# Optimization experiments

Measured on AMD Instinct MI355X. Metric: run time of the kernel, lower is better.

The kernel has to match this reference:

```python
import jax, jax.numpy as jnp
import numpy as np

B, S, D = 256, 64, 512
H, DK, DV = 8, 64, 64
DFF = 2048
IN_SIZE = S * D  # 32768
OUT = 50
EPS = 1e-5


def _layernorm(x, gamma, beta):
    mu = jnp.mean(x, axis=-1, keepdims=True)
    var = jnp.mean((x - mu) ** 2, axis=-1, keepdims=True)
    return (x - mu) * jax.lax.rsqrt(var + EPS) * gamma + beta


def setup_inputs() -> dict:
    key = jax.random.key(0)
    ks = jax.random.split(key, 16)
    s = lambda fan_in: 1.0 / np.sqrt(fan_in)
    inp = {
        "inputs": jax.random.normal(ks[0], (B, S, D), dtype=jnp.float32),
        # per-head projections stacked over heads (concat order preserved)
        "Wq": jax.random.normal(ks[1], (H, D, DK), dtype=jnp.float32) * s(D),
        "bq": jnp.zeros((H, DK), dtype=jnp.float32),
        "Wk": jax.random.normal(ks[2], (H, D, DK), dtype=jnp.float32) * s(D),
        "bk": jnp.zeros((H, DK), dtype=jnp.float32),
        "Wv": jax.random.normal(ks[3], (H, D, DV), dtype=jnp.float32) * s(D),
        "bv": jnp.zeros((H, DV), dtype=jnp.float32),
        "Wo": jax.random.normal(ks[4], (H * DV, D), dtype=jnp.float32) * s(H * DV),
        "bo": jnp.zeros((D,), dtype=jnp.float32),
        "ln1_g": jnp.ones((D,), dtype=jnp.float32),
        "ln1_b": jnp.zeros((D,), dtype=jnp.float32),
        "W1": jax.random.normal(ks[5], (IN_SIZE, DFF), dtype=jnp.float32) * s(IN_SIZE),
        "b1": jnp.zeros((DFF,), dtype=jnp.float32),
        "W2": jax.random.normal(ks[6], (DFF, IN_SIZE), dtype=jnp.float32) * s(DFF),
        "b2": jnp.zeros((IN_SIZE,), dtype=jnp.float32),
        "ln2_g": jnp.ones((IN_SIZE,), dtype=jnp.float32),
        "ln2_b": jnp.zeros((IN_SIZE,), dtype=jnp.float32),
        "Wf": jax.random.normal(ks[7], (IN_SIZE, OUT), dtype=jnp.float32) * s(IN_SIZE),
        "bf": jnp.zeros((OUT,), dtype=jnp.float32),
    }
    return inp


def reference(inputs, Wq, bq, Wk, bk, Wv, bv, Wo, bo, ln1_g, ln1_b,
              W1, b1, W2, b2, ln2_g, ln2_b, Wf, bf):
    # --- multi-head attention (all heads batched via einsum) ---
    q = jnp.einsum('bsd,hdk->bhsk', inputs, Wq) + bq[:, None, :]
    k = jnp.einsum('bsd,hdk->bhsk', inputs, Wk) + bk[:, None, :]
    v = jnp.einsum('bsd,hdv->bhsv', inputs, Wv) + bv[:, None, :]
    scores = jnp.einsum('bhsk,bhtk->bhst', q, k) / jnp.sqrt(jnp.float32(DK))
    attn = jax.nn.softmax(scores, axis=-1)
    ctx = jnp.einsum('bhst,bhtv->bhsv', attn, v)          # [B,H,S,DV]
    ctx = ctx.transpose(0, 2, 1, 3).reshape(B, S, H * DV)  # concat heads
    proj = ctx @ Wo + bo
    hs = _layernorm(inputs + proj, ln1_g, ln1_b)           # [B,S,D]
    # --- flatten + FFN with residual + LN ---
    x = hs.reshape(B, IN_SIZE)
    h = jax.nn.relu(x @ W1 + b1)
    y = _layernorm(h @ W2 + b2 + x, ln2_g, ln2_b)
    # --- final classifier ---
    return y @ Wf + bf
```

## Files before the change

kernel.cpp:

```cpp
#include <hip/hip_runtime.h>

#define BB   256
#define SS   64
#define DD   512
#define HH   8
#define DKK  64
#define BSZ  16384
#define INSZ 32768
#define DFF  2048
#define NOUT 50
#define KSF  128
#define KCF  256

typedef float f32x4 __attribute__((ext_vector_type(4)));
typedef __bf16 bf16x8 __attribute__((ext_vector_type(8)));
typedef unsigned short u16x8 __attribute__((ext_vector_type(8)));

__device__ inline unsigned short f2bf(float f) {
    unsigned u = __builtin_bit_cast(unsigned, f);
    u += 0x7FFFu + ((u >> 16) & 1u);
    return (unsigned short)(u >> 16);
}
__device__ inline bf16x8 ld_frag(const unsigned short* p) {
    return __builtin_bit_cast(bf16x8, *(const u16x8*)p);
}
#define MFMA(a,b,c) __builtin_amdgcn_mfma_f32_16x16x32_bf16(a,b,c,0,0,0)

__global__ __launch_bounds__(256) void k_qkv(
    const float* __restrict__ X,  const float* __restrict__ Wq,
    const float* __restrict__ bq, const float* __restrict__ Wk,
    const float* __restrict__ bk, const float* __restrict__ Wv,
    const float* __restrict__ bv, unsigned short* __restrict__ qkv)
{
    const int mt = blockIdx.x, h = blockIdx.y;
    const int tid = threadIdx.x, wave = tid >> 6, lane = tid & 63;
    const int m0 = mt * 64;
    __shared__ unsigned short Xs[64][72];
    __shared__ unsigned short Ws[192][72];

    const float* Wb0 = Wq + (size_t)h * DD * DKK;
    const float* Wb1 = Wk + (size_t)h * DD * DKK;
    const float* Wb2 = Wv + (size_t)h * DD * DKK;

    f32x4 acc[12] = {};
    for (int k0 = 0; k0 < DD; k0 += 64) {
        for (int p = 0; p < 4; ++p) {
            int e = tid + p * 256;
            int r = e >> 4, c4 = e & 15;
            float4 v = *(const float4*)(X + (size_t)(m0 + r) * DD + k0 + c4 * 4);
            int c = c4 * 4;
            Xs[r][c] = f2bf(v.x); Xs[r][c+1] = f2bf(v.y);
            Xs[r][c+2] = f2bf(v.z); Xs[r][c+3] = f2bf(v.w);
        }
        for (int w3 = 0; w3 < 3; ++w3) {
            const float* W = (w3 == 0) ? Wb0 : (w3 == 1) ? Wb1 : Wb2;
            for (int p = 0; p < 4; ++p) {
                int e = tid + p * 256;
                int kr = e >> 4, c4 = e & 15;
                float4 v = *(const float4*)(W + (size_t)(k0 + kr) * DKK + c4 * 4);
                int nb = w3 * 64 + c4 * 4;
                Ws[nb][kr] = f2bf(v.x); Ws[nb+1][kr] = f2bf(v.y);
                Ws[nb+2][kr] = f2bf(v.z); Ws[nb+3][kr] = f2bf(v.w);
            }
        }
        __syncthreads();
        for (int ks = 0; ks < 64; ks += 32) {
            bf16x8 a = ld_frag(&Xs[wave*16 + (lane & 15)][ks + (lane >> 4) * 8]);
            for (int nt = 0; nt < 12; ++nt) {
                bf16x8 b = ld_frag(&Ws[nt*16 + (lane & 15)][ks + (lane >> 4) * 8]);
                acc[nt] = MFMA(a, b, acc[nt]);
            }
        }
        __syncthreads();
    }
    for (int nt = 0; nt < 12; ++nt) {
        int w3 = nt >> 2;
        const float* bias = ((w3 == 0) ? bq : (w3 == 1) ? bk : bv) + h * DKK;
        float scale = (w3 == 0) ? 0.125f : 1.0f;
        unsigned short* out = qkv + ((size_t)(w3 * BB + mt) * HH + h) * (SS * DKK);
        for (int r = 0; r < 4; ++r) {
            int s = wave * 16 + (lane >> 4) * 4 + r;
            int c = (nt & 3) * 16 + (lane & 15);
            out[s * DKK + c] = f2bf((acc[nt][r] + bias[c]) * scale);
        }
    }
}

__global__ __launch_bounds__(256) void k_attn(
    const unsigned short* __restrict__ qkv, unsigned short* __restrict__ ctx)
{
    const int b = blockIdx.x >> 3, h = blockIdx.x & 7;
    const int tid = threadIdx.x, wave = tid >> 6, lane = tid & 63;
    __shared__ unsigned short Qs[64][72], Ks[64][72], Vt[64][72], Ps[64][72];

    const unsigned short* qp = qkv + ((size_t)(0 * BB + b) * HH + h) * 4096;
    const unsigned short* kp = qkv + ((size_t)(1 * BB + b) * HH + h) * 4096;
    const unsigned short* vp = qkv + ((size_t)(2 * BB + b) * HH + h) * 4096;

    for (int p = 0; p < 4; ++p) {
        int e = tid + p * 256;
        int r = e >> 4, c4 = (e & 15) * 4;
        *(ushort4*)&Qs[r][c4] = *(const ushort4*)(qp + r * 64 + c4);
        *(ushort4*)&Ks[r][c4] = *(const ushort4*)(kp + r * 64 + c4);
    }
    for (int p = 0; p < 16; ++p) {
        int e = tid + p * 256;
        int t = e >> 6, dv = e & 63;
        Vt[dv][t] = vp[t * 64 + dv];
    }
    __syncthreads();

    f32x4 sa[4] = {};
    for (int ks = 0; ks < 64; ks += 32) {
        bf16x8 a = ld_frag(&Qs[wave*16 + (lane & 15)][ks + (lane >> 4) * 8]);
        for (int nt = 0; nt < 4; ++nt) {
            bf16x8 bb = ld_frag(&Ks[nt*16 + (lane & 15)][ks + (lane >> 4) * 8]);
            sa[nt] = MFMA(a, bb, sa[nt]);
        }
    }
    for (int r = 0; r < 4; ++r) {
        float mx = fmaxf(fmaxf(sa[0][r], sa[1][r]), fmaxf(sa[2][r], sa[3][r]));
        for (int off = 1; off < 16; off <<= 1) mx = fmaxf(mx, __shfl_xor(mx, off, 64));
        float e0 = __expf(sa[0][r] - mx), e1 = __expf(sa[1][r] - mx);
        float e2 = __expf(sa[2][r] - mx), e3 = __expf(sa[3][r] - mx);
        float sm = e0 + e1 + e2 + e3;
        for (int off = 1; off < 16; off <<= 1) sm += __shfl_xor(sm, off, 64);
        float inv = 1.f / sm;
        sa[0][r] = e0 * inv; sa[1][r] = e1 * inv; sa[2][r] = e2 * inv; sa[3][r] = e3 * inv;
    }
    for (int nt = 0; nt < 4; ++nt)
        for (int r = 0; r < 4; ++r)
            Ps[wave*16 + (lane >> 4) * 4 + r][nt*16 + (lane & 15)] = f2bf(sa[nt][r]);
    __syncthreads();

    f32x4 oa[4] = {};
    for (int ks = 0; ks < 64; ks += 32) {
        bf16x8 a = ld_frag(&Ps[wave*16 + (lane & 15)][ks + (lane >> 4) * 8]);
        for (int nt = 0; nt < 4; ++nt) {
            bf16x8 bb = ld_frag(&Vt[nt*16 + (lane & 15)][ks + (lane >> 4) * 8]);
            oa[nt] = MFMA(a, bb, oa[nt]);
        }
    }
    unsigned short* cp = ctx + (size_t)b * SS * DD + h * DKK;
    for (int nt = 0; nt < 4; ++nt)
        for (int r = 0; r < 4; ++r) {
            int s = wave * 16 + (lane >> 4) * 4 + r;
            int dv = nt * 16 + (lane & 15);
            cp[(size_t)s * DD + dv] = f2bf(oa[nt][r]);
        }
}

__global__ __launch_bounds__(256) void k_oproj(
    const unsigned short* __restrict__ ctx, const float* __restrict__ Wo,
    const float* __restrict__ bo, const float* __restrict__ X,
    float* __restrict__ t1)
{
    const int mt = blockIdx.x, n0 = blockIdx.y * 128;
    const int tid = threadIdx.x, wave = tid >> 6, lane = tid & 63;
    const int m0 = mt * 64;
    __shared__ unsigned short As[64][72], Bs[128][72];
    f32x4 acc[8] = {};
    for (int k0 = 0; k0 < DD; k0 += 64) {
        for (int p = 0; p < 4; ++p) {
            int e = tid + p * 256; int r = e >> 4, c4 = (e & 15) * 4;
            *(ushort4*)&As[r][c4] = *(const ushort4*)(ctx + (size_t)(m0 + r) * DD + k0 + c4);
        }
        for (int p = 0; p < 8; ++p) {
            int e = tid + p * 256; int kr = e >> 5, c4 = e & 31;
            float4 v = *(const float4*)(Wo + (size_t)(k0 + kr) * DD + n0 + c4 * 4);
            int nb = c4 * 4;
            Bs[nb][kr] = f2bf(v.x); Bs[nb+1][kr] = f2bf(v.y);
            Bs[nb+2][kr] = f2bf(v.z); Bs[nb+3][kr] = f2bf(v.w);
        }
        __syncthreads();
        for (int ks = 0; ks < 64; ks += 32) {
            bf16x8 a = ld_frag(&As[wave*16 + (lane & 15)][ks + (lane >> 4) * 8]);
            for (int nt = 0; nt < 8; ++nt) {
                bf16x8 bb = ld_frag(&Bs[nt*16 + (lane & 15)][ks + (lane >> 4) * 8]);
                acc[nt] = MFMA(a, bb, acc[nt]);
            }
        }
        __syncthreads();
    }
    for (int nt = 0; nt < 8; ++nt)
        for (int r = 0; r < 4; ++r) {
            int m = m0 + wave * 16 + (lane >> 4) * 4 + r;
            int n = n0 + nt * 16 + (lane & 15);
            t1[(size_t)m * DD + n] = acc[nt][r] + bo[n] + X[(size_t)m * DD + n];
        }
}

__global__ __launch_bounds__(256) void k_ln1(
    float* __restrict__ t1, const float* __restrict__ g,
    const float* __restrict__ bv, unsigned short* __restrict__ hs16)
{
    const int tid = threadIdx.x, wave = tid >> 6, lane = tid & 63;
    const int row = blockIdx.x * 4 + wave;
    float* p = t1 + (size_t)row * DD;
    float4 v0 = *(const float4*)(p + lane * 4);
    float4 v1 = *(const float4*)(p + 256 + lane * 4);
    float s = v0.x + v0.y + v0.z + v0.w + v1.x + v1.y + v1.z + v1.w;
    float q = v0.x*v0.x + v0.y*v0.y + v0.z*v0.z + v0.w*v0.w
            + v1.x*v1.x + v1.y*v1.y + v1.z*v1.z + v1.w*v1.w;
    for (int off = 1; off < 64; off <<= 1) { s += __shfl_xor(s, off, 64); q += __shfl_xor(q, off, 64); }
    float mu = s / DD;
    float rs = rsqrtf(q / DD - mu * mu + 1e-5f);
    float4 g0 = *(const float4*)(g + lane * 4), g1 = *(const float4*)(g + 256 + lane * 4);
    float4 b0 = *(const float4*)(bv + lane * 4), b1 = *(const float4*)(bv + 256 + lane * 4);
    float4 o0, o1;
    o0.x = (v0.x - mu) * rs * g0.x + b0.x; o0.y = (v0.y - mu) * rs * g0.y + b0.y;
    o0.z = (v0.z - mu) * rs * g0.z + b0.z; o0.w = (v0.w - mu) * rs * g0.w + b0.w;
    o1.x = (v1.x - mu) * rs * g1.x + b1.x; o1.y = (v1.y - mu) * rs * g1.y + b1.y;
    o1.z = (v1.z - mu) * rs * g1.z + b1.z; o1.w = (v1.w - mu) * rs * g1.w + b1.w;
    *(float4*)(p + lane * 4) = o0;
    *(float4*)(p + 256 + lane * 4) = o1;
    unsigned short* hp = hs16 + (size_t)row * DD;
    ushort4 u;
    u.x = f2bf(o0.x); u.y = f2bf(o0.y); u.z = f2bf(o0.z); u.w = f2bf(o0.w);
    *(ushort4*)(hp + lane * 4) = u;
    u.x = f2bf(o1.x); u.y = f2bf(o1.y); u.z = f2bf(o1.z); u.w = f2bf(o1.w);
    *(ushort4*)(hp + 256 + lane * 4) = u;
}

__global__ __launch_bounds__(256) void k_ffn1(
    const unsigned short* __restrict__ hs16, const float* __restrict__ W1,
    float* __restrict__ part)
{
    const int n0 = blockIdx.x * 64, kbase = blockIdx.y * 2048;
    const int tid = threadIdx.x, wave = tid >> 6, lane = tid & 63;
    __shared__ unsigned short As[256][72], Bs[64][72];
    f32x4 acc[4][4] = {};
    for (int kc = 0; kc < 2048; kc += 64) {
        int k0 = kbase + kc;
        for (int p = 0; p < 16; ++p) {
            int e = tid + p * 256; int r = e >> 4, c4 = (e & 15) * 4;
            *(ushort4*)&As[r][c4] = *(const ushort4*)(hs16 + (size_t)r * INSZ + k0 + c4);
        }
        for (int p = 0; p < 4; ++p) {
            int e = tid + p * 256; int kr = e >> 4, c4 = e & 15;
            float4 v = *(const float4*)(W1 + (size_t)(k0 + kr) * DFF + n0 + c4 * 4);
            int nb = c4 * 4;
            Bs[nb][kr] = f2bf(v.x); Bs[nb+1][kr] = f2bf(v.y);
            Bs[nb+2][kr] = f2bf(v.z); Bs[nb+3][kr] = f2bf(v.w);
        }
        __syncthreads();
        for (int ks = 0; ks < 64; ks += 32) {
            bf16x8 bfr[4];
            for (int nt = 0; nt < 4; ++nt)
                bfr[nt] = ld_frag(&Bs[nt*16 + (lane & 15)][ks + (lane >> 4) * 8]);
            for (int mt2 = 0; mt2 < 4; ++mt2) {
                bf16x8 a = ld_frag(&As[wave*64 + mt2*16 + (lane & 15)][ks + (lane >> 4) * 8]);
                for (int nt = 0; nt < 4; ++nt) acc[mt2][nt] = MFMA(a, bfr[nt], acc[mt2][nt]);
            }
        }
        __syncthreads();
    }
    float* pp = part + (size_t)blockIdx.y * 256 * DFF;
    for (int mt2 = 0; mt2 < 4; ++mt2)
        for (int nt = 0; nt < 4; ++nt)
            for (int r = 0; r < 4; ++r) {
                int m = wave * 64 + mt2 * 16 + (lane >> 4) * 4 + r;
                int n = n0 + nt * 16 + (lane & 15);
                pp[(size_t)m * DFF + n] = acc[mt2][nt][r];
            }
}

__global__ __launch_bounds__(256) void k_ffn1red(
    const float* __restrict__ part, const float* __restrict__ b1,
    unsigned short* __restrict__ h16)
{
    int e = blockIdx.x * 256 + threadIdx.x;
    int m = e >> 9;
    int c = (e & 511) * 4;
    float4 s = {0.f, 0.f, 0.f, 0.f};
    for (int p = 0; p < 16; ++p) {
        float4 v = *(const float4*)(part + ((size_t)p * 256 + m) * DFF + c);
        s.x += v.x; s.y += v.y; s.z += v.z; s.w += v.w;
    }
    float4 bb = *(const float4*)(b1 + c);
    s.x = fmaxf(s.x + bb.x, 0.f); s.y = fmaxf(s.y + bb.y, 0.f);
    s.z = fmaxf(s.z + bb.z, 0.f); s.w = fmaxf(s.w + bb.w, 0.f);
    ushort4 u; u.x = f2bf(s.x); u.y = f2bf(s.y); u.z = f2bf(s.z); u.w = f2bf(s.w);
    *(ushort4*)(h16 + (size_t)m * DFF + c) = u;
}

__global__ __launch_bounds__(256) void k_ffn2(
    const unsigned short* __restrict__ h16, const float* __restrict__ W2,
    const float* __restrict__ b2, const float* __restrict__ hs32,
    float* __restrict__ t2)
{
    const int n0 = blockIdx.x * 64;
    const int tid = threadIdx.x, wave = tid >> 6, lane = tid & 63;
    __shared__ unsigned short As[256][72], Bs[64][72];
    f32x4 acc[4][4] = {};
    for (int k0 = 0; k0 < DFF; k0 += 64) {
        for (int p = 0; p < 16; ++p) {
            int e = tid + p * 256; int r = e >> 4, c4 = (e & 15) * 4;
            *(ushort4*)&As[r][c4] = *(const ushort4*)(h16 + (size_t)r * DFF + k0 + c4);
        }
        for (int p = 0; p < 4; ++p) {
            int e = tid + p * 256; int kr = e >> 4, c4 = e & 15;
            float4 v = *(const float4*)(W2 + (size_t)(k0 + kr) * INSZ + n0 + c4 * 4);
            int nb = c4 * 4;
            Bs[nb][kr] = f2bf(v.x); Bs[nb+1][kr] = f2bf(v.y);
            Bs[nb+2][kr] = f2bf(v.z); Bs[nb+3][kr] = f2bf(v.w);
        }
        __syncthreads();
        for (int ks = 0; ks < 64; ks += 32) {
            bf16x8 bfr[4];
            for (int nt = 0; nt < 4; ++nt)
                bfr[nt] = ld_frag(&Bs[nt*16 + (lane & 15)][ks + (lane >> 4) * 8]);
            for (int mt2 = 0; mt2 < 4; ++mt2) {
                bf16x8 a = ld_frag(&As[wave*64 + mt2*16 + (lane & 15)][ks + (lane >> 4) * 8]);
                for (int nt = 0; nt < 4; ++nt) acc[mt2][nt] = MFMA(a, bfr[nt], acc[mt2][nt]);
            }
        }
        __syncthreads();
    }
    for (int mt2 = 0; mt2 < 4; ++mt2)
        for (int nt = 0; nt < 4; ++nt)
            for (int r = 0; r < 4; ++r) {
                int m = wave * 64 + mt2 * 16 + (lane >> 4) * 4 + r;
                int n = n0 + nt * 16 + (lane & 15);
                size_t idx = (size_t)m * INSZ + n;
                t2[idx] = acc[mt2][nt][r] + b2[n] + hs32[idx];
            }
}

__global__ __launch_bounds__(256) void k_ln2stats(
    const float* __restrict__ t2, float* __restrict__ stats)
{
    const int m = blockIdx.x, tid = threadIdx.x;
    const float* p = t2 + (size_t)m * INSZ;
    float s = 0.f, q = 0.f;
    for (int i = tid; i < INSZ / 4; i += 256) {
        float4 v = *(const float4*)(p + i * 4);
        s += v.x + v.y + v.z + v.w;
        q += v.x*v.x + v.y*v.y + v.z*v.z + v.w*v.w;
    }
    for (int off = 1; off < 64; off <<= 1) { s += __shfl_xor(s, off, 64); q += __shfl_xor(q, off, 64); }
    __shared__ float ss[4], qq[4];
    if ((tid & 63) == 0) { ss[tid >> 6] = s; qq[tid >> 6] = q; }
    __syncthreads();
    if (tid == 0) {
        s = ss[0] + ss[1] + ss[2] + ss[3];
        q = qq[0] + qq[1] + qq[2] + qq[3];
        float mu = s / INSZ;
        stats[m * 2] = mu;
        stats[m * 2 + 1] = rsqrtf(q / INSZ - mu * mu + 1e-5f);
    }
}

__global__ __launch_bounds__(256) void k_fgemm(
    const float* __restrict__ t2, const float* __restrict__ g,
    const float* __restrict__ bv, const float* __restrict__ Wf,
    float* __restrict__ fpart)
{
    const int sp = blockIdx.x, kbase = sp * KCF;
    const int tid = threadIdx.x, wave = tid >> 6, lane = tid & 63;
    __shared__ unsigned short As[272][72], Bs[64][72];
    f32x4 acc[5][4] = {};
    for (int kc = 0; kc < KCF; kc += 64) {
        int k0 = kbase + kc;
        for (int p = 0; p < 68; ++p) {
            int e = tid + p * 256;
            int r = e >> 6, c = e & 63;
            int k = k0 + c;
            float val;
            if (r < 256)      val = t2[(size_t)r * INSZ + k] * g[k];
            else if (r == 256) val = g[k];
            else if (r == 257) val = bv[k];
            else               val = 0.f;
            As[r][c] = f2bf(val);
        }
        for (int p = 0; p < 16; ++p) {
            int e = tid + p * 256;
            int kr = e >> 6, n = e & 63;
            Bs[n][kr] = (n < NOUT) ? f2bf(Wf[(size_t)(k0 + kr) * NOUT + n]) : (unsigned short)0;
        }
        __syncthreads();
        for (int ks = 0; ks < 64; ks += 32) {
            bf16x8 bfr[4];
            for (int nt = 0; nt < 4; ++nt)
                bfr[nt] = ld_frag(&Bs[nt*16 + (lane & 15)][ks + (lane >> 4) * 8]);
            int i = 0;
            for (int mt = wave; mt < 17; mt += 4, ++i) {
                bf16x8 a = ld_frag(&As[mt*16 + (lane & 15)][ks + (lane >> 4) * 8]);
                for (int nt = 0; nt < 4; ++nt) acc[i][nt] = MFMA(a, bfr[nt], acc[i][nt]);
            }
        }
        __syncthreads();
    }
    float* pp = fpart + (size_t)sp * 272 * 64;
    int i = 0;
    for (int mt = wave; mt < 17; mt += 4, ++i)
        for (int nt = 0; nt < 4; ++nt)
            for (int r = 0; r < 4; ++r) {
                int m = mt * 16 + (lane >> 4) * 4 + r;
                int n = nt * 16 + (lane & 15);
                pp[m * 64 + n] = acc[i][nt][r];
            }
}

__global__ __launch_bounds__(64) void k_fout(
    const float* __restrict__ fpart, const float* __restrict__ stats,
    const float* __restrict__ bf_, float* __restrict__ out)
{
    const int m = blockIdx.x, n = threadIdx.x;
    float s = 0.f, sg = 0.f, sb = 0.f;
    for (int sp = 0; sp < KSF; ++sp) {
        const float* pp = fpart + (size_t)sp * 272 * 64;
        s  += pp[m * 64 + n];
        sg += pp[256 * 64 + n];
        sb += pp[257 * 64 + n];
    }
    if (n < NOUT) {
        float mu = stats[m * 2], rs = stats[m * 2 + 1];
        out[m * NOUT + n] = rs * (s - mu * sg) + sb + bf_[n];
    }
}

extern "C" void kernel_launch(void* const* d_in, const int* in_sizes, int n_in,
                              void* d_out, int out_size, void* d_ws, size_t ws_size,
                              hipStream_t stream) {
    const float* X   = (const float*)d_in[0];
    const float* Wq  = (const float*)d_in[1];
    const float* bq  = (const float*)d_in[2];
    const float* Wk  = (const float*)d_in[3];
    const float* bk  = (const float*)d_in[4];
    const float* Wv  = (const float*)d_in[5];
    const float* bv  = (const float*)d_in[6];
    const float* Wo  = (const float*)d_in[7];
    const float* bo  = (const float*)d_in[8];
    const float* g1  = (const float*)d_in[9];
    const float* b1v = (const float*)d_in[10];
    const float* W1  = (const float*)d_in[11];
    const float* b1  = (const float*)d_in[12];
    const float* W2  = (const float*)d_in[13];
    const float* b2  = (const float*)d_in[14];
    const float* g2  = (const float*)d_in[15];
    const float* b2v = (const float*)d_in[16];
    const float* Wf  = (const float*)d_in[17];
    const float* bfv = (const float*)d_in[18];
    float* out = (float*)d_out;
    char* ws = (char*)d_ws;

    unsigned short* qkv  = (unsigned short*)(ws + 0);
    float* part1         = (float*)(ws + 0);
    float* fpart         = (float*)(ws + 0);
    unsigned short* hs16 = (unsigned short*)(ws + 33554432);
    unsigned short* ctx  = (unsigned short*)(ws + 50331648);
    float* t2            = (float*)(ws + 50331648);
    float* t1            = (float*)(ws + 83886080);
    unsigned short* h16  = (unsigned short*)(ws + 117440512);
    float* stats         = (float*)(ws + 118489088);

    k_qkv<<<dim3(256, 8), 256, 0, stream>>>(X, Wq, bq, Wk, bk, Wv, bv, qkv);
    k_attn<<<2048, 256, 0, stream>>>(qkv, ctx);
    k_oproj<<<dim3(256, 4), 256, 0, stream>>>(ctx, Wo, bo, X, t1);
    k_ln1<<<4096, 256, 0, stream>>>(t1, g1, b1v, hs16);
    k_ffn1<<<dim3(32, 16), 256, 0, stream>>>(hs16, W1, part1);
    k_ffn1red<<<512, 256, 0, stream>>>(part1, b1, h16);
    k_ffn2<<<512, 256, 0, stream>>>(h16, W2, b2, t1, t2);
    k_ln2stats<<<256, 256, 0, stream>>>(t2, stats);
    k_fgemm<<<KSF, 256, 0, stream>>>(t2, g2, b2v, Wf, fpart);
    k_fout<<<256, 64, 0, stream>>>(fpart, stats, bfv, out);
}
```

Baseline: 1.029 ms.

## Swizzle LDS tiles, retile QKV/oproj GEMMs, pre-convert X, rework final split-K

```diff
diff --git a/kernel.cpp b/kernel.cpp
--- a/kernel.cpp
+++ b/kernel.cpp
@@ -9,8 +9,8 @@
 #define INSZ 32768
 #define DFF  2048
 #define NOUT 50
-#define KSF  128
-#define KCF  256
+#define KSF  256
+#define KCF  128
 
 typedef float f32x4 __attribute__((ext_vector_type(4)));
 typedef __bf16 bf16x8 __attribute__((ext_vector_type(8)));
@@ -26,64 +26,93 @@
 }
 #define MFMA(a,b,c) __builtin_amdgcn_mfma_f32_16x16x32_bf16(a,b,c,0,0,0)
 
+__device__ inline int sw(int row, int col) {
+    return row * 64 + ((((col >> 3) ^ (row & 7)) << 3) | (col & 7));
+}
+
+__device__ inline void stage_w64(const float* __restrict__ W, int ldn,
+                                 unsigned short* Bs, int tid) {
+    const int n = tid & 63, wq = tid >> 6;
+    #pragma unroll
+    for (int p = 0; p < 2; ++p) {
+        const int k0 = wq * 8 + p * 32;
+        const float* src = W + (size_t)k0 * ldn + n;
+        unsigned short tmp[8];
+        #pragma unroll
+        for (int j = 0; j < 8; ++j) tmp[j] = f2bf(src[(size_t)j * ldn]);
+        *(u16x8*)&Bs[sw(n, k0)] = *(const u16x8*)tmp;
+    }
+}
+
+__device__ inline void stage_a256(const unsigned short* __restrict__ src, int lds_,
+                                  unsigned short* As, int tid) {
+    #pragma unroll
+    for (int p = 0; p < 8; ++p) {
+        int e = tid + p * 256;
+        int r = e >> 3, c8 = (e & 7) * 8;
+        u16x8 v = *(const u16x8*)(src + (size_t)r * lds_ + c8);
+        *(u16x8*)&As[sw(r, c8)] = v;
+    }
+}
+
+__global__ __launch_bounds__(256) void k_x16(
+    const float* __restrict__ X, unsigned short* __restrict__ x16)
+{
+    int e = blockIdx.x * 256 + threadIdx.x;
+    float4 v = ((const float4*)X)[e];
+    ushort4 u;
+    u.x = f2bf(v.x); u.y = f2bf(v.y); u.z = f2bf(v.z); u.w = f2bf(v.w);
+    ((ushort4*)x16)[e] = u;
+}
+
 __global__ __launch_bounds__(256) void k_qkv(
-    const float* __restrict__ X,  const float* __restrict__ Wq,
-    const float* __restrict__ bq, const float* __restrict__ Wk,
-    const float* __restrict__ bk, const float* __restrict__ Wv,
-    const float* __restrict__ bv, unsigned short* __restrict__ qkv)
-{
-    const int mt = blockIdx.x, h = blockIdx.y;
-    const int tid = threadIdx.x, wave = tid >> 6, lane = tid & 63;
-    const int m0 = mt * 64;
-    __shared__ unsigned short Xs[64][72];
-    __shared__ unsigned short Ws[192][72];
-
-    const float* Wb0 = Wq + (size_t)h * DD * DKK;
-    const float* Wb1 = Wk + (size_t)h * DD * DKK;
-    const float* Wb2 = Wv + (size_t)h * DD * DKK;
-
-    f32x4 acc[12] = {};
+    const unsigned short* __restrict__ x16,
+    const float* __restrict__ Wq, const float* __restrict__ bq,
+    const float* __restrict__ Wk, const float* __restrict__ bk,
+    const float* __restrict__ Wv, const float* __restrict__ bv,
+    unsigned short* __restrict__ qkv)
+{
+    const int m0 = blockIdx.x * 256;
+    const int nt = blockIdx.y, w3 = nt >> 3, h = nt & 7;
+    const int tid = threadIdx.x, wave = tid >> 6, lane = tid & 63;
+    const float* Wbase = ((w3 == 0) ? Wq : (w3 == 1) ? Wk : Wv) + (size_t)h * DD * DKK;
+    __shared__ __align__(16) unsigned short As[256 * 64];
+    __shared__ __align__(16) unsigned short Bs[64 * 64];
+
+    f32x4 acc[4][4] = {};
     for (int k0 = 0; k0 < DD; k0 += 64) {
-        for (int p = 0; p < 4; ++p) {
-            int e = tid + p * 256;
-            int r = e >> 4, c4 = e & 15;
-            float4 v = *(const float4*)(X + (size_t)(m0 + r) * DD + k0 + c4 * 4);
-            int c = c4 * 4;
-            Xs[r][c] = f2bf(v.x); Xs[r][c+1] = f2bf(v.y);
-            Xs[r][c+2] = f2bf(v.z); Xs[r][c+3] = f2bf(v.w);
-        }
-        for (int w3 = 0; w3 < 3; ++w3) {
-            const float* W = (w3 == 0) ? Wb0 : (w3 == 1) ? Wb1 : Wb2;
-            for (int p = 0; p < 4; ++p) {
-                int e = tid + p * 256;
-                int kr = e >> 4, c4 = e & 15;
-                float4 v = *(const float4*)(W + (size_t)(k0 + kr) * DKK + c4 * 4);
-                int nb = w3 * 64 + c4 * 4;
-                Ws[nb][kr] = f2bf(v.x); Ws[nb+1][kr] = f2bf(v.y);
-                Ws[nb+2][kr] = f2bf(v.z); Ws[nb+3][kr] = f2bf(v.w);
-            }
-        }
-        __syncthreads();
+        stage_a256(x16 + (size_t)m0 * DD + k0, DD, As, tid);
+        stage_w64(Wbase + (size_t)k0 * DKK, DKK, Bs, tid);
+        __syncthreads();
+        #pragma unroll
         for (int ks = 0; ks < 64; ks += 32) {
-            bf16x8 a = ld_frag(&Xs[wave*16 + (lane & 15)][ks + (lane >> 4) * 8]);
-            for (int nt = 0; nt < 12; ++nt) {
-                bf16x8 b = ld_frag(&Ws[nt*16 + (lane & 15)][ks + (lane >> 4) * 8]);
-                acc[nt] = MFMA(a, b, acc[nt]);
-            }
-        }
-        __syncthreads();
-    }
-    for (int nt = 0; nt < 12; ++nt) {
-        int w3 = nt >> 2;
-        const float* bias = ((w3 == 0) ? bq : (w3 == 1) ? bk : bv) + h * DKK;
-        float scale = (w3 == 0) ? 0.125f : 1.0f;
-        unsigned short* out = qkv + ((size_t)(w3 * BB + mt) * HH + h) * (SS * DKK);
-        for (int r = 0; r < 4; ++r) {
-            int s = wave * 16 + (lane >> 4) * 4 + r;
-            int c = (nt & 3) * 16 + (lane & 15);
-            out[s * DKK + c] = f2bf((acc[nt][r] + bias[c]) * scale);
-        }
-    }
+            bf16x8 bfr[4];
+            #pragma unroll
+            for (int n2 = 0; n2 < 4; ++n2)
+                bfr[n2] = ld_frag(&Bs[sw(n2*16 + (lane & 15), ks + (lane >> 4) * 8)]);
+            #pragma unroll
+            for (int m2 = 0; m2 < 4; ++m2) {
+                bf16x8 a = ld_frag(&As[sw(wave*64 + m2*16 + (lane & 15), ks + (lane >> 4) * 8)]);
+                #pragma unroll
+                for (int n2 = 0; n2 < 4; ++n2) acc[m2][n2] = MFMA(a, bfr[n2], acc[m2][n2]);
+            }
+        }
+        __syncthreads();
+    }
+    const float* bias = ((w3 == 0) ? bq : (w3 == 1) ? bk : bv) + h * DKK;
+    const float scale = (w3 == 0) ? 0.125f : 1.0f;
+    #pragma unroll
+    for (int m2 = 0; m2 < 4; ++m2)
+        #pragma unroll
+        for (int n2 = 0; n2 < 4; ++n2)
+            #pragma unroll
+            for (int r = 0; r < 4; ++r) {
+                int m = m0 + wave*64 + m2*16 + (lane >> 4) * 4 + r;
+                int b = m >> 6, s = m & 63;
+                int dk = n2*16 + (lane & 15);
+                qkv[((size_t)(w3 * BB + b) * HH + h) * 4096 + s * 64 + dk]
+                    = f2bf((acc[m2][n2][r] + bias[dk]) * scale);
+            }
 }
 
 __global__ __launch_bounds__(256) void k_attn(
@@ -91,33 +120,40 @@
 {
     const int b = blockIdx.x >> 3, h = blockIdx.x & 7;
     const int tid = threadIdx.x, wave = tid >> 6, lane = tid & 63;
-    __shared__ unsigned short Qs[64][72], Ks[64][72], Vt[64][72], Ps[64][72];
+    __shared__ __align__(16) unsigned short Qs[64*64], Ks[64*64], Vt[64*64], Ps[64*64];
 
     const unsigned short* qp = qkv + ((size_t)(0 * BB + b) * HH + h) * 4096;
     const unsigned short* kp = qkv + ((size_t)(1 * BB + b) * HH + h) * 4096;
     const unsigned short* vp = qkv + ((size_t)(2 * BB + b) * HH + h) * 4096;
 
-    for (int p = 0; p < 4; ++p) {
+    #pragma unroll
+    for (int p = 0; p < 2; ++p) {
         int e = tid + p * 256;
-        int r = e >> 4, c4 = (e & 15) * 4;
-        *(ushort4*)&Qs[r][c4] = *(const ushort4*)(qp + r * 64 + c4);
-        *(ushort4*)&Ks[r][c4] = *(const ushort4*)(kp + r * 64 + c4);
-    }
-    for (int p = 0; p < 16; ++p) {
-        int e = tid + p * 256;
-        int t = e >> 6, dv = e & 63;
-        Vt[dv][t] = vp[t * 64 + dv];
+        int r = e >> 3, c8 = (e & 7) * 8;
+        *(u16x8*)&Qs[sw(r, c8)] = *(const u16x8*)(qp + r * 64 + c8);
+        *(u16x8*)&Ks[sw(r, c8)] = *(const u16x8*)(kp + r * 64 + c8);
+    }
+    {
+        int dv = tid & 63, tb = (tid >> 6) * 16;
+        unsigned short tmp[16];
+        #pragma unroll
+        for (int i = 0; i < 16; ++i) tmp[i] = vp[(tb + i) * 64 + dv];
+        *(u16x8*)&Vt[sw(dv, tb)]     = *(const u16x8*)&tmp[0];
+        *(u16x8*)&Vt[sw(dv, tb + 8)] = *(const u16x8*)&tmp[8];
     }
     __syncthreads();
 
     f32x4 sa[4] = {};
+    #pragma unroll
     for (int ks = 0; ks < 64; ks += 32) {
-        bf16x8 a = ld_frag(&Qs[wave*16 + (lane & 15)][ks + (lane >> 4) * 8]);
-        for (int nt = 0; nt < 4; ++nt) {
-            bf16x8 bb = ld_frag(&Ks[nt*16 + (lane & 15)][ks + (lane >> 4) * 8]);
-            sa[nt] = MFMA(a, bb, sa[nt]);
-        }
-    }
+        bf16x8 a = ld_frag(&Qs[sw(wave*16 + (lane & 15), ks + (lane >> 4) * 8)]);
+        #pragma unroll
+        for (int n2 = 0; n2 < 4; ++n2) {
+            bf16x8 bb = ld_frag(&Ks[sw(n2*16 + (lane & 15), ks + (lane >> 4) * 8)]);
+            sa[n2] = MFMA(a, bb, sa[n2]);
+        }
+    }
+    #pragma unroll
     for (int r = 0; r < 4; ++r) {
         float mx = fmaxf(fmaxf(sa[0][r], sa[1][r]), fmaxf(sa[2][r], sa[3][r]));
         for (int off = 1; off < 16; off <<= 1) mx = fmaxf(mx, __shfl_xor(mx, off, 64));
@@ -128,25 +164,30 @@
         float inv = 1.f / sm;
         sa[0][r] = e0 * inv; sa[1][r] = e1 * inv; sa[2][r] = e2 * inv; sa[3][r] = e3 * inv;
     }
-    for (int nt = 0; nt < 4; ++nt)
+    #pragma unroll
+    for (int n2 = 0; n2 < 4; ++n2)
+        #pragma unroll
         for (int r = 0; r < 4; ++r)
-            Ps[wave*16 + (lane >> 4) * 4 + r][nt*16 + (lane & 15)] = f2bf(sa[nt][r]);
+            Ps[sw(wave*16 + (lane >> 4)*4 + r, n2*16 + (lane & 15))] = f2bf(sa[n2][r]);
     __syncthreads();
 
     f32x4 oa[4] = {};
+    #pragma unroll
     for (int ks = 0; ks < 64; ks += 32) {
-        bf16x8 a = ld_frag(&Ps[wave*16 + (lane & 15)][ks + (lane >> 4) * 8]);
-        for (int nt = 0; nt < 4; ++nt) {
-            bf16x8 bb = ld_frag(&Vt[nt*16 + (lane & 15)][ks + (lane >> 4) * 8]);
-            oa[nt] = MFMA(a, bb, oa[nt]);
+        bf16x8 a = ld_frag(&Ps[sw(wave*16 + (lane & 15), ks + (lane >> 4) * 8)]);
+        #pragma unroll
+        for (int n2 = 0; n2 < 4; ++n2) {
+            bf16x8 bb = ld_frag(&Vt[sw(n2*16 + (lane & 15), ks + (lane >> 4) * 8)]);
+            oa[n2] = MFMA(a, bb, oa[n2]);
         }
     }
     unsigned short* cp = ctx + (size_t)b * SS * DD + h * DKK;
-    for (int nt = 0; nt < 4; ++nt)
+    #pragma unroll
+    for (int n2 = 0; n2 < 4; ++n2)
+        #pragma unroll
         for (int r = 0; r < 4; ++r) {
-            int s = wave * 16 + (lane >> 4) * 4 + r;
-            int dv = nt * 16 + (lane & 15);
-            cp[(size_t)s * DD + dv] = f2bf(oa[nt][r]);
+            int s = wave*16 + (lane >> 4)*4 + r;
+            cp[(size_t)s * DD + n2*16 + (lane & 15)] = f2bf(oa[n2][r]);
         }
 }
 
@@ -155,39 +196,40 @@
     const float* __restrict__ bo, const float* __restrict__ X,
     float* __restrict__ t1)
 {
-    const int mt = blockIdx.x, n0 = blockIdx.y * 128;
-    const int tid = threadIdx.x, wave = tid >> 6, lane = tid & 63;
-    const int m0 = mt * 64;
-    __shared__ unsigned short As[64][72], Bs[128][72];
-    f32x4 acc[8] = {};
+    const int m0 = blockIdx.x * 256, n0 = blockIdx.y * 64;
+    const int tid = threadIdx.x, wave = tid >> 6, lane = tid & 63;
+    __shared__ __align__(16) unsigned short As[256 * 64];
+    __shared__ __align__(16) unsigned short Bs[64 * 64];
+    f32x4 acc[4][4] = {};
     for (int k0 = 0; k0 < DD; k0 += 64) {
-        for (int p = 0; p < 4; ++p) {
-            int e = tid + p * 256; int r = e >> 4, c4 = (e & 15) * 4;
-            *(ushort4*)&As[r][c4] = *(const ushort4*)(ctx + (size_t)(m0 + r) * DD + k0 + c4);
-        }
-        for (int p = 0; p < 8; ++p) {
-            int e = tid + p * 256; int kr = e >> 5, c4 = e & 31;
-            float4 v = *(const float4*)(Wo + (size_t)(k0 + kr) * DD + n0 + c4 * 4);
-            int nb = c4 * 4;
-            Bs[nb][kr] = f2bf(v.x); Bs[nb+1][kr] = f2bf(v.y);
-            Bs[nb+2][kr] = f2bf(v.z); Bs[nb+3][kr] = f2bf(v.w);
-        }
-        __syncthreads();
+        stage_a256(ctx + (size_t)m0 * DD + k0, DD, As, tid);
+        stage_w64(Wo + (size_t)k0 * DD + n0, DD, Bs, tid);
+        __syncthreads();
+        #pragma unroll
         for (int ks = 0; ks < 64; ks += 32) {
-            bf16x8 a = ld_frag(&As[wave*16 + (lane & 15)][ks + (lane >> 4) * 8]);
-            for (int nt = 0; nt < 8; ++nt) {
-                bf16x8 bb = ld_frag(&Bs[nt*16 + (lane & 15)][ks + (lane >> 4) * 8]);
-                acc[nt] = MFMA(a, bb, acc[nt]);
-            }
-        }
-        __syncthreads();
-    }
-    for (int nt = 0; nt < 8; ++nt)
-        for (int r = 0; r < 4; ++r) {
-            int m = m0 + wave * 16 + (lane >> 4) * 4 + r;
-            int n = n0 + nt * 16 + (lane & 15);
-            t1[(size_t)m * DD + n] = acc[nt][r] + bo[n] + X[(size_t)m * DD + n];
-        }
+            bf16x8 bfr[4];
+            #pragma unroll
+            for (int n2 = 0; n2 < 4; ++n2)
+                bfr[n2] = ld_frag(&Bs[sw(n2*16 + (lane & 15), ks + (lane >> 4) * 8)]);
+            #pragma unroll
+            for (int m2 = 0; m2 < 4; ++m2) {
+                bf16x8 a = ld_frag(&As[sw(wave*64 + m2*16 + (lane & 15), ks + (lane >> 4) * 8)]);
+                #pragma unroll
+                for (int n2 = 0; n2 < 4; ++n2) acc[m2][n2] = MFMA(a, bfr[n2], acc[m2][n2]);
+            }
+        }
+        __syncthreads();
+    }
+    #pragma unroll
+    for (int m2 = 0; m2 < 4; ++m2)
+        #pragma unroll
+        for (int n2 = 0; n2 < 4; ++n2)
+            #pragma unroll
+            for (int r = 0; r < 4; ++r) {
+                int m = m0 + wave*64 + m2*16 + (lane >> 4)*4 + r;
+                int n = n0 + n2*16 + (lane & 15);
+                t1[(size_t)m * DD + n] = acc[m2][n2][r] + bo[n] + X[(size_t)m * DD + n];
+            }
 }
 
 __global__ __launch_bounds__(256) void k_ln1(
@@ -228,40 +270,39 @@
 {
     const int n0 = blockIdx.x * 64, kbase = blockIdx.y * 2048;
     const int tid = threadIdx.x, wave = tid >> 6, lane = tid & 63;
-    __shared__ unsigned short As[256][72], Bs[64][72];
+    __shared__ __align__(16) unsigned short As[256 * 64];
+    __shared__ __align__(16) unsigned short Bs[64 * 64];
     f32x4 acc[4][4] = {};
     for (int kc = 0; kc < 2048; kc += 64) {
         int k0 = kbase + kc;
-        for (int p = 0; p < 16; ++p) {
-            int e = tid + p * 256; int r = e >> 4, c4 = (e & 15) * 4;
-            *(ushort4*)&As[r][c4] = *(const ushort4*)(hs16 + (size_t)r * INSZ + k0 + c4);
-        }
-        for (int p = 0; p < 4; ++p) {
-            int e = tid + p * 256; int kr = e >> 4, c4 = e & 15;
-            float4 v = *(const float4*)(W1 + (size_t)(k0 + kr) * DFF + n0 + c4 * 4);
-            int nb = c4 * 4;
-            Bs[nb][kr] = f2bf(v.x); Bs[nb+1][kr] = f2bf(v.y);
-            Bs[nb+2][kr] = f2bf(v.z); Bs[nb+3][kr] = f2bf(v.w);
-        }
-        __syncthreads();
+        stage_a256(hs16 + k0, INSZ, As, tid);
+        stage_w64(W1 + (size_t)k0 * DFF + n0, DFF, Bs, tid);
+        __syncthreads();
+        #pragma unroll
         for (int ks = 0; ks < 64; ks += 32) {
             bf16x8 bfr[4];
-            for (int nt = 0; nt < 4; ++nt)
-                bfr[nt] = ld_frag(&Bs[nt*16 + (lane & 15)][ks + (lane >> 4) * 8]);
-            for (int mt2 = 0; mt2 < 4; ++mt2) {
-                bf16x8 a = ld_frag(&As[wave*64 + mt2*16 + (lane & 15)][ks + (lane >> 4) * 8]);
-                for (int nt = 0; nt < 4; ++nt) acc[mt2][nt] = MFMA(a, bfr[nt], acc[mt2][nt]);
+            #pragma unroll
+            for (int n2 = 0; n2 < 4; ++n2)
+                bfr[n2] = ld_frag(&Bs[sw(n2*16 + (lane & 15), ks + (lane >> 4) * 8)]);
+            #pragma unroll
+            for (int m2 = 0; m2 < 4; ++m2) {
+                bf16x8 a = ld_frag(&As[sw(wave*64 + m2*16 + (lane & 15), ks + (lane >> 4) * 8)]);
+                #pragma unroll
+                for (int n2 = 0; n2 < 4; ++n2) acc[m2][n2] = MFMA(a, bfr[n2], acc[m2][n2]);
             }
         }
         __syncthreads();
     }
     float* pp = part + (size_t)blockIdx.y * 256 * DFF;
-    for (int mt2 = 0; mt2 < 4; ++mt2)
-        for (int nt = 0; nt < 4; ++nt)
+    #pragma unroll
+    for (int m2 = 0; m2 < 4; ++m2)
+        #pragma unroll
+        for (int n2 = 0; n2 < 4; ++n2)
+            #pragma unroll
             for (int r = 0; r < 4; ++r) {
-                int m = wave * 64 + mt2 * 16 + (lane >> 4) * 4 + r;
-                int n = n0 + nt * 16 + (lane & 15);
-                pp[(size_t)m * DFF + n] = acc[mt2][nt][r];
+                int m = wave*64 + m2*16 + (lane >> 4)*4 + r;
+                int n = n0 + n2*16 + (lane & 15);
+                pp[(size_t)m * DFF + n] = acc[m2][n2][r];
             }
 }
 
@@ -291,39 +332,38 @@
 {
     const int n0 = blockIdx.x * 64;
     const int tid = threadIdx.x, wave = tid >> 6, lane = tid & 63;
-    __shared__ unsigned short As[256][72], Bs[64][72];
+    __shared__ __align__(16) unsigned short As[256 * 64];
+    __shared__ __align__(16) unsigned short Bs[64 * 64];
     f32x4 acc[4][4] = {};
     for (int k0 = 0; k0 < DFF; k0 += 64) {
-        for (int p = 0; p < 16; ++p) {
-            int e = tid + p * 256; int r = e >> 4, c4 = (e & 15) * 4;
-            *(ushort4*)&As[r][c4] = *(const ushort4*)(h16 + (size_t)r * DFF + k0 + c4);
-        }
-        for (int p = 0; p < 4; ++p) {
-            int e = tid + p * 256; int kr = e >> 4, c4 = e & 15;
-            float4 v = *(const float4*)(W2 + (size_t)(k0 + kr) * INSZ + n0 + c4 * 4);
-            int nb = c4 * 4;
-            Bs[nb][kr] = f2bf(v.x); Bs[nb+1][kr] = f2bf(v.y);
-            Bs[nb+2][kr] = f2bf(v.z); Bs[nb+3][kr] = f2bf(v.w);
-        }
-        __syncthreads();
+        stage_a256(h16 + k0, DFF, As, tid);
+        stage_w64(W2 + (size_t)k0 * INSZ + n0, INSZ, Bs, tid);
+        __syncthreads();
+        #pragma unroll
         for (int ks = 0; ks < 64; ks += 32) {
             bf16x8 bfr[4];
-            for (int nt = 0; nt < 4; ++nt)
-                bfr[nt] = ld_frag(&Bs[nt*16 + (lane & 15)][ks + (lane >> 4) * 8]);
-            for (int mt2 = 0; mt2 < 4; ++mt2) {
-                bf16x8 a = ld_frag(&As[wave*64 + mt2*16 + (lane & 15)][ks + (lane >> 4) * 8]);
-                for (int nt = 0; nt < 4; ++nt) acc[mt2][nt] = MFMA(a, bfr[nt], acc[mt2][nt]);
-            }
-        }
-        __syncthreads();
-    }
-    for (int mt2 = 0; mt2 < 4; ++mt2)
-        for (int nt = 0; nt < 4; ++nt)
+            #pragma unroll
+            for (int n2 = 0; n2 < 4; ++n2)
+                bfr[n2] = ld_frag(&Bs[sw(n2*16 + (lane & 15), ks + (lane >> 4) * 8)]);
+            #pragma unroll
+            for (int m2 = 0; m2 < 4; ++m2) {
+                bf16x8 a = ld_frag(&As[sw(wave*64 + m2*16 + (lane & 15), ks + (lane >> 4) * 8)]);
+                #pragma unroll
+                for (int n2 = 0; n2 < 4; ++n2) acc[m2][n2] = MFMA(a, bfr[n2], acc[m2][n2]);
+            }
+        }
+        __syncthreads();
+    }
+    #pragma unroll
+    for (int m2 = 0; m2 < 4; ++m2)
+        #pragma unroll
+        for (int n2 = 0; n2 < 4; ++n2)
+            #pragma unroll
             for (int r = 0; r < 4; ++r) {
-                int m = wave * 64 + mt2 * 16 + (lane >> 4) * 4 + r;
-                int n = n0 + nt * 16 + (lane & 15);
+                int m = wave*64 + m2*16 + (lane >> 4)*4 + r;
+                int n = n0 + n2*16 + (lane & 15);
                 size_t idx = (size_t)m * INSZ + n;
-                t2[idx] = acc[mt2][nt][r] + b2[n] + hs32[idx];
+                t2[idx] = acc[m2][n2][r] + b2[n] + hs32[idx];
             }
 }
 
@@ -358,7 +398,8 @@
 {
     const int sp = blockIdx.x, kbase = sp * KCF;
     const int tid = threadIdx.x, wave = tid >> 6, lane = tid & 63;
-    __shared__ unsigned short As[272][72], Bs[64][72];
+    __shared__ __align__(16) unsigned short As[272][72];
+    __shared__ __align__(16) unsigned short Bs[64 * 64];
     f32x4 acc[5][4] = {};
     for (int kc = 0; kc < KCF; kc += 64) {
         int k0 = kbase + kc;
@@ -367,56 +408,73 @@
             int r = e >> 6, c = e & 63;
             int k = k0 + c;
             float val;
-            if (r < 256)      val = t2[(size_t)r * INSZ + k] * g[k];
+            if (r < 256)       val = t2[(size_t)r * INSZ + k] * g[k];
             else if (r == 256) val = g[k];
             else if (r == 257) val = bv[k];
             else               val = 0.f;
             As[r][c] = f2bf(val);
         }
-        for (int p = 0; p < 16; ++p) {
-            int e = tid + p * 256;
-            int kr = e >> 6, n = e & 63;
-            Bs[n][kr] = (n < NOUT) ? f2bf(Wf[(size_t)(k0 + kr) * NOUT + n]) : (unsigned short)0;
-        }
-        __syncthreads();
+        {
+            int n = tid & 63, wq = tid >> 6;
+            #pragma unroll
+            for (int p = 0; p < 2; ++p) {
+                int kk = wq * 8 + p * 32;
+                unsigned short tmp[8];
+                #pragma unroll
+                for (int j = 0; j < 8; ++j)
+                    tmp[j] = (n < NOUT) ? f2bf(Wf[(size_t)(k0 + kk + j) * NOUT + n]) : (unsigned short)0;
+                *(u16x8*)&Bs[sw(n, kk)] = *(const u16x8*)tmp;
+            }
+        }
+        __syncthreads();
+        #pragma unroll
         for (int ks = 0; ks < 64; ks += 32) {
             bf16x8 bfr[4];
-            for (int nt = 0; nt < 4; ++nt)
-                bfr[nt] = ld_frag(&Bs[nt*16 + (lane & 15)][ks + (lane >> 4) * 8]);
+            #pragma unroll
+            for (int n2 = 0; n2 < 4; ++n2)
+                bfr[n2] = ld_frag(&Bs[sw(n2*16 + (lane & 15), ks + (lane >> 4) * 8)]);
             int i = 0;
             for (int mt = wave; mt < 17; mt += 4, ++i) {
                 bf16x8 a = ld_frag(&As[mt*16 + (lane & 15)][ks + (lane >> 4) * 8]);
-                for (int nt = 0; nt < 4; ++nt) acc[i][nt] = MFMA(a, bfr[nt], acc[i][nt]);
-            }
-        }
-        __syncthreads();
-    }
-    float* pp = fpart + (size_t)sp * 272 * 64;
+                #pragma unroll
+                for (int n2 = 0; n2 < 4; ++n2) acc[i][n2] = MFMA(a, bfr[n2], acc[i][n2]);
+            }
+        }
+        __syncthreads();
+    }
     int i = 0;
     for (int mt = wave; mt < 17; mt += 4, ++i)
-        for (int nt = 0; nt < 4; ++nt)
+        #pragma unroll
+        for (int n2 = 0; n2 < 4; ++n2)
+            #pragma unroll
             for (int r = 0; r < 4; ++r) {
-                int m = mt * 16 + (lane >> 4) * 4 + r;
-                int n = nt * 16 + (lane & 15);
-                pp[m * 64 + n] = acc[i][nt][r];
-            }
-}
-
-__global__ __launch_bounds__(64) void k_fout(
+                int m = mt*16 + (lane >> 4)*4 + r;
+                int n = n2*16 + (lane & 15);
+                fpart[((size_t)m * KSF + sp) * 64 + n] = acc[i][n2][r];
+            }
+}
+
+__global__ __launch_bounds__(256) void k_fout(
     const float* __restrict__ fpart, const float* __restrict__ stats,
     const float* __restrict__ bf_, float* __restrict__ out)
 {
-    const int m = blockIdx.x, n = threadIdx.x;
+    const int m = blockIdx.x, tid = threadIdx.x;
+    const int n = tid & 63, sq = tid >> 6;
     float s = 0.f, sg = 0.f, sb = 0.f;
-    for (int sp = 0; sp < KSF; ++sp) {
-        const float* pp = fpart + (size_t)sp * 272 * 64;
-        s  += pp[m * 64 + n];
-        sg += pp[256 * 64 + n];
-        sb += pp[257 * 64 + n];
-    }
-    if (n < NOUT) {
-        float mu = stats[m * 2], rs = stats[m * 2 + 1];
-        out[m * NOUT + n] = rs * (s - mu * sg) + sb + bf_[n];
+    for (int sp = sq * 64; sp < sq * 64 + 64; ++sp) {
+        s  += fpart[((size_t)m   * KSF + sp) * 64 + n];
+        sg += fpart[((size_t)256 * KSF + sp) * 64 + n];
+        sb += fpart[((size_t)257 * KSF + sp) * 64 + n];
+    }
+    __shared__ float red[3][4][64];
+    red[0][sq][n] = s; red[1][sq][n] = sg; red[2][sq][n] = sb;
+    __syncthreads();
+    if (tid < NOUT) {
+        float S  = red[0][0][tid] + red[0][1][tid] + red[0][2][tid] + red[0][3][tid];
+        float SG = red[1][0][tid] + red[1][1][tid] + red[1][2][tid] + red[1][3][tid];
+        float SB = red[2][0][tid] + red[2][1][tid] + red[2][2][tid] + red[2][3][tid];
+        float mu = stats[m * 2], rv = stats[m * 2 + 1];
+        out[m * NOUT + tid] = rv * (S - mu * SG) + SB + bf_[tid];
     }
 }
 
@@ -445,24 +503,26 @@
     float* out = (float*)d_out;
     char* ws = (char*)d_ws;
 
-    unsigned short* qkv  = (unsigned short*)(ws + 0);
-    float* part1         = (float*)(ws + 0);
-    float* fpart         = (float*)(ws + 0);
-    unsigned short* hs16 = (unsigned short*)(ws + 33554432);
-    unsigned short* ctx  = (unsigned short*)(ws + 50331648);
-    float* t2            = (float*)(ws + 50331648);
+    unsigned short* x16  = (unsigned short*)(ws + 0);
+    unsigned short* qkv  = (unsigned short*)(ws + 16777216);
+    unsigned short* ctx  = (unsigned short*)(ws + 67108864);
     float* t1            = (float*)(ws + 83886080);
-    unsigned short* h16  = (unsigned short*)(ws + 117440512);
-    float* stats         = (float*)(ws + 118489088);
-
-    k_qkv<<<dim3(256, 8), 256, 0, stream>>>(X, Wq, bq, Wk, bk, Wv, bv, qkv);
+    unsigned short* hs16 = (unsigned short*)(ws + 0);
+    float* part1         = (float*)(ws + 16777216);
+    unsigned short* h16  = (unsigned short*)(ws + 50331648);
+    float* t2            = (float*)(ws + 0);
+    float* fpart         = (float*)(ws + 33554432);
+    float* stats         = (float*)(ws + 51380224);
+
+    k_x16<<<8192, 256, 0, stream>>>(X, x16);
+    k_qkv<<<dim3(64, 24), 256, 0, stream>>>(x16, Wq, bq, Wk, bk, Wv, bv, qkv);
     k_attn<<<2048, 256, 0, stream>>>(qkv, ctx);
-    k_oproj<<<dim3(256, 4), 256, 0, stream>>>(ctx, Wo, bo, X, t1);
+    k_oproj<<<dim3(64, 8), 256, 0, stream>>>(ctx, Wo, bo, X, t1);
     k_ln1<<<4096, 256, 0, stream>>>(t1, g1, b1v, hs16);
     k_ffn1<<<dim3(32, 16), 256, 0, stream>>>(hs16, W1, part1);
     k_ffn1red<<<512, 256, 0, stream>>>(part1, b1, h16);
     k_ffn2<<<512, 256, 0, stream>>>(h16, W2, b2, t1, t2);
     k_ln2stats<<<256, 256, 0, stream>>>(t2, stats);
     k_fgemm<<<KSF, 256, 0, stream>>>(t2, g2, b2v, Wf, fpart);
-    k_fout<<<256, 64, 0, stream>>>(fpart, stats, bfv, out);
-}
+    k_fout<<<256, 256, 0, stream>>>(fpart, stats, bfv, out);
+}
```

New measurement: 844.6 us. 17.9% less time.
